# Kernel optimization log

Measured on AMD Instinct MI355X. Metric: run time of the kernel, lower is better.

The kernel has to match this reference:

```python
import jax, jax.numpy as jnp
import numpy as np

ALPHA = 2.0   # spikingjelly surrogate.ATan default alpha
TAU = 2.0
VTH = 1.0
EPS = 1e-5

@jax.custom_vjp
def atan_spike(x):
    return (x >= 0.0).astype(x.dtype)

def _as_fwd(x):
    return atan_spike(x), x

def _as_bwd(x, g):
    # ATan surrogate derivative: alpha/2 / (1 + (pi/2*alpha*x)^2)
    return (g * (ALPHA / 2.0) / (1.0 + (jnp.pi / 2.0 * ALPHA * x) ** 2),)

atan_spike.defvjp(_as_fwd, _as_bwd)

def lif_multistep(x):
    # x: [B, T, D]; LIF with decay_input=True, v_reset=0 (hard reset), detach_reset=True
    xt = jnp.swapaxes(x, 0, 1)  # [T, B, D] time-major
    def step(v, xi):
        v = v + (xi - v) / TAU                       # integrate with input decay
        s = atan_spike(v - VTH)                       # fire (surrogate grad)
        v = v * (1.0 - jax.lax.stop_gradient(s))      # hard reset to 0, detached
        return v, s
    _, spikes = jax.lax.scan(step, jnp.zeros_like(xt[0]), xt)
    return jnp.swapaxes(spikes, 0, 1)  # [B, T, D]

def layernorm(x, g, b):
    m = x.mean(-1, keepdims=True)
    v = x.var(-1, keepdims=True)
    return (x - m) / jnp.sqrt(v + EPS) * g + b

def setup_inputs() -> dict:
    key = jax.random.key(0)
    ks = jax.random.split(key, 6)
    B, T, IN, HP, E, H, D = 256, 256, 4, 64, 512, 1024, 4
    s = 0.02
    return {
        "hist_feat": jax.random.normal(ks[0], (B, T, IN), jnp.float32),
        "pW1": jax.random.normal(ks[1], (IN, HP), jnp.float32) * s,
        "pb1": jnp.zeros((HP,), jnp.float32),
        "pW2": jax.random.normal(ks[2], (HP, E), jnp.float32) * s,
        "pb2": jnp.zeros((E,), jnp.float32),
        "fc1_w": jax.random.normal(ks[3], (D, E, H), jnp.float32) * s,
        "fc1_b": jnp.zeros((D, H), jnp.float32),
        "ln1_g": jnp.ones((D, H), jnp.float32),
        "ln1_b": jnp.zeros((D, H), jnp.float32),
        "fc2_w": jax.random.normal(ks[4], (D, H, E), jnp.float32) * s,
        "fc2_b": jnp.zeros((D, E), jnp.float32),
        "ln2_g": jnp.ones((D, E), jnp.float32),
        "ln2_b": jnp.zeros((D, E), jnp.float32),
    }

def reference(hist_feat, pW1, pb1, pW2, pb2, fc1_w, fc1_b, ln1_g, ln1_b,
              fc2_w, fc2_b, ln2_g, ln2_b):
    # input projector: Linear -> exact GELU -> Linear
    x = jax.nn.gelu(hist_feat @ pW1 + pb1, approximate=False) @ pW2 + pb2  # [B,T,E]
    depth = fc1_w.shape[0]
    for d in range(depth):  # small fixed layer loop
        res = x
        h = layernorm(x @ fc1_w[d] + fc1_b[d], ln1_g[d], ln1_b[d])  # [B,T,H]
        h = lif_multistep(h)
        h = layernorm(h @ fc2_w[d] + fc2_b[d], ln2_g[d], ln2_b[d])  # [B,T,E]
        h = lif_multistep(h)
        x = res + h  # dropout is identity in eval mode
    return x[:, -1]  # pooling='last', no mask -> last timestep, [B,E]
```

## Files before the change

### kernel.cpp

```cpp
#include <hip/hip_runtime.h>
#include <hip/hip_bf16.h>
#include <math.h>

#define B_  256
#define T_  256
#define IN_ 4
#define HP_ 64
#define E_  512
#define H_  1024
#define D_  4

typedef __hip_bfloat16 bf16;
typedef _Float16 f16;
typedef _Float16 f16x8 __attribute__((ext_vector_type(8)));
typedef float f32x4 __attribute__((ext_vector_type(4)));

__device__ __forceinline__ float load1(const void* p, size_t idx, bool isb) {
    if (isb) {
        unsigned int u = ((const unsigned short*)p)[idx];
        return __uint_as_float(u << 16);
    }
    return ((const float*)p)[idx];
}

__device__ __forceinline__ float4 load4(const void* p, size_t idx, bool isb) {
    if (isb) {
        ushort4 u = *(const ushort4*)((const unsigned short*)p + idx);
        float4 r;
        r.x = __uint_as_float(((unsigned int)u.x) << 16);
        r.y = __uint_as_float(((unsigned int)u.y) << 16);
        r.z = __uint_as_float(((unsigned int)u.z) << 16);
        r.w = __uint_as_float(((unsigned int)u.w) << 16);
        return r;
    }
    return *((const float4*)p + (idx >> 2));
}

__device__ __forceinline__ void split3(float x, f16& h, f16& hs, f16& lb) {
    h = (f16)x;
    float hf = (float)h;
    hs = (f16)(hf * 4.8828125e-4f);
    lb = (f16)((x - hf) * 2048.0f);
}

__global__ void sniff_count_kernel(const unsigned short* __restrict__ p,
                                   int* __restrict__ cnts) {
    __shared__ int cnt;
    if (threadIdx.x == 0) cnt = 0;
    __syncthreads();
    int local = 0;
    #pragma unroll
    for (int k = 0; k < 4; ++k) {
        int i = blockIdx.x * 1024 + k * 256 + threadIdx.x;
        unsigned int bits = ((unsigned int)p[i]) << 16;
        float v = __uint_as_float(bits);
        float a = fabsf(v);
        if (!(a <= 1e4f)) local++;
        else if (v != 0.0f && a < 1e-6f) local++;
    }
    atomicAdd(&cnt, local);
    __syncthreads();
    if (threadIdx.x == 0) cnts[blockIdx.x] = cnt;
}

__global__ void sniff_final_kernel(const int* __restrict__ cnts,
                                   int* __restrict__ flag) {
    int s = 0;
    for (int i = 0; i < 64; ++i) s += cnts[i];
    *flag = (s > 1024) ? 0 : 1;
}

__global__ __launch_bounds__(256) void wsplit_kernel(
        const void* __restrict__ W, size_t wOff, unsigned short* __restrict__ Wt,
        int K, int N, const int* __restrict__ flag) {
    const bool isb = (*flag != 0);
    __shared__ float tile[32][33];
    const int n0 = blockIdx.x * 32, k0 = blockIdx.y * 32;
    const int t = threadIdx.x;
    {
        int lk = t >> 3, ln0 = (t & 7) << 2;
        float4 v = load4(W, wOff + (size_t)(k0 + lk) * N + n0 + ln0, isb);
        tile[lk][ln0 + 0] = v.x; tile[lk][ln0 + 1] = v.y;
        tile[lk][ln0 + 2] = v.z; tile[lk][ln0 + 3] = v.w;
    }
    __syncthreads();
    int n = t >> 3, kq0 = (t & 7) << 2;
    size_t base = (size_t)(n0 + n) * (2 * (size_t)K) + k0 + kq0;
    #pragma unroll
    for (int j = 0; j < 4; ++j) {
        float x = tile[kq0 + j][n];
        f16 h, hs, lb;
        split3(x, h, hs, lb);
        Wt[base + j]     = *(unsigned short*)&h;
        Wt[base + j + K] = *(unsigned short*)&lb;
    }
}

template<int NPL>
__device__ __forceinline__ void gemm_mfma_body(
        const unsigned short* __restrict__ At, const unsigned short* __restrict__ Wt,
        const void* __restrict__ bias, size_t bOff,
        float* __restrict__ C, int N, int K, const int* __restrict__ flag) {
    const bool isb = (*flag != 0);
    constexpr int APL = (NPL == 3) ? 2 : 1;
    __shared__ unsigned short As[2][128 * 64];
    __shared__ unsigned short Bs[2][128 * 64];

    const int gx = N >> 7;
    const int gy = (int)gridDim.x / gx;
    int bx, by;
    {
        int bid = blockIdx.x;
        if ((gy & 7) == 0) {
            int k = bid & 7, i = bid >> 3;
            bx = i % gx;
            by = (gy >> 3) * k + i / gx;
        } else { bx = bid % gx; by = bid / gx; }
    }
    const int bn = bx * 128;
    const int bm = by * 128;

    const int tid  = threadIdx.x;
    const int lane = tid & 63;
    const int wave = tid >> 6;
    const int wm = wave >> 1;
    const int wn = wave & 1;
    const int g  = lane >> 4;
    const int lr = lane & 15;

    const int sar = tid >> 1;
    const int sah = tid & 1;
    const int sbn = tid >> 1;
    const int sq  = tid & 1;

    const f16 C11 = (f16)4.8828125e-4f;
    const f16x8 c11v = {C11, C11, C11, C11, C11, C11, C11, C11};

    f32x4 acc[4][4];
    #pragma unroll
    for (int i = 0; i < 4; ++i)
        #pragma unroll
        for (int j = 0; j < 4; ++j) acc[i][j] = (f32x4){0.f, 0.f, 0.f, 0.f};

    const unsigned short* Ap = At + (size_t)(bm + sar) * (APL * (size_t)K) + sah * 16;
    const unsigned short* Wp = Wt + (size_t)(bn + sbn) * (2 * (size_t)K) + sq * 16;

    f16x8 av[2 * APL], wv[4];
    #pragma unroll
    for (int pl = 0; pl < APL; ++pl)
        #pragma unroll
        for (int c = 0; c < 2; ++c)
            av[pl * 2 + c] = *(const f16x8*)(Ap + (size_t)pl * K + c * 8);
    #pragma unroll
    for (int pl = 0; pl < 2; ++pl)
        #pragma unroll
        for (int c = 0; c < 2; ++c)
            wv[pl * 2 + c] = *(const f16x8*)(Wp + (size_t)pl * K + c * 8);

    const int nt = K >> 5;
    for (int t = 0; t < nt; ++t) {
        const int cur = t & 1;
        const int arb = sar * 64, asw = sar & 7;
        #pragma unroll
        for (int pl = 0; pl < APL; ++pl)
            #pragma unroll
            for (int c = 0; c < 2; ++c) {
                const int gg = sah * 2 + c;
                *(f16x8*)&As[cur][arb + (((pl << 2) | gg) ^ asw) * 8] = av[pl * 2 + c];
            }
        const int brb = sbn * 64, bsw = sbn & 7;
        #pragma unroll
        for (int pl = 0; pl < 2; ++pl)
            #pragma unroll
            for (int c = 0; c < 2; ++c) {
                const int gg = sq * 2 + c;
                *(f16x8*)&Bs[cur][brb + (((pl << 2) | gg) ^ bsw) * 8] = wv[pl * 2 + c];
            }
        __syncthreads();
        if (t + 1 < nt) {
            const int k0 = (t + 1) << 5;
            #pragma unroll
            for (int pl = 0; pl < APL; ++pl)
                #pragma unroll
                for (int c = 0; c < 2; ++c)
                    av[pl * 2 + c] = *(const f16x8*)(Ap + (size_t)pl * K + k0 + c * 8);
            #pragma unroll
            for (int pl = 0; pl < 2; ++pl)
                #pragma unroll
                for (int c = 0; c < 2; ++c)
                    wv[pl * 2 + c] = *(const f16x8*)(Wp + (size_t)pl * K + k0 + c * 8);
        }
        f16x8 a0[4], b0[4], b2[4], a2[4];
        #pragma unroll
        for (int mi = 0; mi < 4; ++mi) {
            const int ar = wm * 64 + mi * 16 + lr;
            a0[mi] = *(const f16x8*)&As[cur][ar * 64 + ((g ^ (ar & 7))) * 8];
            if (NPL == 3)
                a2[mi] = *(const f16x8*)&As[cur][ar * 64 + (((4 | g) ^ (ar & 7))) * 8];
        }
        #pragma unroll
        for (int ni = 0; ni < 4; ++ni) {
            const int br = wn * 64 + ni * 16 + lr;
            b0[ni] = *(const f16x8*)&Bs[cur][br * 64 + ((g ^ (br & 7))) * 8];
            b2[ni] = *(const f16x8*)&Bs[cur][br * 64 + (((4 | g) ^ (br & 7))) * 8];
        }
        #pragma unroll
        for (int mi = 0; mi < 4; ++mi)
            #pragma unroll
            for (int ni = 0; ni < 4; ++ni)
                acc[mi][ni] = __builtin_amdgcn_mfma_f32_16x16x32_f16(
                    a0[mi], b0[ni], acc[mi][ni], 0, 0, 0);
        {
            f16x8 a1[4];
            #pragma unroll
            for (int mi = 0; mi < 4; ++mi) a1[mi] = a0[mi] * c11v;
            #pragma unroll
            for (int mi = 0; mi < 4; ++mi)
                #pragma unroll
                for (int ni = 0; ni < 4; ++ni)
                    acc[mi][ni] = __builtin_amdgcn_mfma_f32_16x16x32_f16(
                        a1[mi], b2[ni], acc[mi][ni], 0, 0, 0);
        }
        if (NPL == 3) {
            f16x8 b1[4];
            #pragma unroll
            for (int ni = 0; ni < 4; ++ni) b1[ni] = b0[ni] * c11v;
            #pragma unroll
            for (int mi = 0; mi < 4; ++mi)
                #pragma unroll
                for (int ni = 0; ni < 4; ++ni)
                    acc[mi][ni] = __builtin_amdgcn_mfma_f32_16x16x32_f16(
                        a2[mi], b1[ni], acc[mi][ni], 0, 0, 0);
        }
    }
    #pragma unroll
    for (int ni = 0; ni < 4; ++ni) {
        const int col = bn + wn * 64 + ni * 16 + lr;
        const float bv = load1(bias, bOff + col, isb);
        #pragma unroll
        for (int mi = 0; mi < 4; ++mi) {
            #pragma unroll
            for (int r = 0; r < 4; ++r) {
                const size_t row = (size_t)(bm + wm * 64 + mi * 16 + g * 4 + r);
                C[row * N + col] = acc[mi][ni][r] + bv;
            }
        }
    }
}

__global__ __launch_bounds__(256, 3) void gemm_mfma3_kernel(
        const unsigned short* __restrict__ At, const unsigned short* __restrict__ Wt,
        const void* __restrict__ bias, size_t bOff,
        float* __restrict__ C, int N, int K, const int* __restrict__ flag) {
    gemm_mfma_body<3>(At, Wt, bias, bOff, C, N, K, flag);
}

__global__ __launch_bounds__(256, 3) void gemm_mfma2_kernel(
        const unsigned short* __restrict__ At, const unsigned short* __restrict__ Wt,
        const void* __restrict__ bias, size_t bOff,
        float* __restrict__ C, int N, int K, const int* __restrict__ flag) {
    gemm_mfma_body<2>(At, Wt, bias, bOff, C, N, K, flag);
}

#define RB_ 16
__global__ __launch_bounds__(256) void proj_kernel(
        const void* __restrict__ hist, const void* __restrict__ pW1,
        const void* __restrict__ pb1,  const void* __restrict__ pW2,
        const void* __restrict__ pb2,  float* __restrict__ Xc,
        unsigned short* __restrict__ At1,
        size_t m0, const int* __restrict__ flag) {
    const bool isb = (*flag != 0);
    __shared__ float h1[RB_][HP_];
    const size_t mb = (size_t)blockIdx.x * RB_;
    const int tid = threadIdx.x;
    const int lane = tid & 63;
    const int grp = tid >> 6;
    #pragma unroll
    for (int rep = 0; rep < 4; ++rep) {
        int idx = tid + rep * 256;
        int r = idx >> 6, c = idx & 63;
        size_t gm = m0 + mb + r;
        float acc = 0.f;
        #pragma unroll
        for (int i = 0; i < IN_; ++i)
            acc = fmaf(load1(hist, gm * IN_ + i, isb),
                       load1(pW1, (size_t)i * HP_ + c, isb), acc);
        acc += load1(pb1, c, isb);
        h1[r][c] = 0.5f * acc * (1.0f + erff(acc * 0.70710678118654752440f));
    }
    __syncthreads();
    const int e0 = lane * 8;
    float acc[4][8];
    #pragma unroll
    for (int r = 0; r < 4; ++r)
        #pragma unroll
        for (int j = 0; j < 8; ++j) acc[r][j] = 0.f;
    for (int i = 0; i < HP_; ++i) {
        float4 wA = load4(pW2, (size_t)i * E_ + e0, isb);
        float4 wB = load4(pW2, (size_t)i * E_ + e0 + 4, isb);
        float w[8] = {wA.x, wA.y, wA.z, wA.w, wB.x, wB.y, wB.z, wB.w};
        #pragma unroll
        for (int r = 0; r < 4; ++r) {
            float h = h1[grp * 4 + r][i];
            #pragma unroll
            for (int j = 0; j < 8; ++j) acc[r][j] = fmaf(h, w[j], acc[r][j]);
        }
    }
    #pragma unroll
    for (int r = 0; r < 4; ++r) {
        size_t row = mb + grp * 4 + r;
        float o[8];
        #pragma unroll
        for (int j = 0; j < 8; ++j)
            o[j] = acc[r][j] + load1(pb2, e0 + j, isb);
        *(float4*)(Xc + row * E_ + e0)     = (float4){o[0], o[1], o[2], o[3]};
        *(float4*)(Xc + row * E_ + e0 + 4) = (float4){o[4], o[5], o[6], o[7]};
        f16x8 hv, lv;
        #pragma unroll
        for (int j = 0; j < 8; ++j) {
            f16 h, hs, lb;
            split3(o[j], h, hs, lb);
            hv[j] = h; lv[j] = lb;
        }
        *(f16x8*)&At1[row * (2 * E_) + e0]      = hv;
        *(f16x8*)&At1[row * (2 * E_) + E_ + e0] = lv;
    }
}

__device__ __forceinline__ float block_sum(float v, float* smem, int tid) {
    #pragma unroll
    for (int off = 32; off > 0; off >>= 1) v += __shfl_down(v, off, 64);
    __syncthreads();
    if ((tid & 63) == 0) smem[tid >> 6] = v;
    __syncthreads();
    if (tid == 0) smem[4] = smem[0] + smem[1] + smem[2] + smem[3];
    __syncthreads();
    return smem[4];
}

__global__ __launch_bounds__(256) void ln_stats_kernel(const float* __restrict__ Y,
                                                       float* __restrict__ stats,
                                                       int N) {
    __shared__ float smem[5];
    size_t row = blockIdx.x;
    const float* y = Y + row * (size_t)N;
    int tid = threadIdx.x;
    int nPer = N >> 8;
    float vals[4];
    float s = 0.f;
    for (int i = 0; i < nPer; ++i) { float v = y[tid + (i << 8)]; vals[i] = v; s += v; }
    float mean = block_sum(s, smem, tid) / (float)N;
    float sq = 0.f;
    for (int i = 0; i < nPer; ++i) { float d0 = vals[i] - mean; sq += d0 * d0; }
    float var = block_sum(sq, smem, tid) / (float)N;
    if (tid == 0) {
        stats[row * 2]     = mean;
        stats[row * 2 + 1] = sqrtf(var + 1e-5f);
    }
}

__global__ __launch_bounds__(64) void lif_kernel(const float* __restrict__ Y,
                                                 const float* __restrict__ stats,
                                                 const void* __restrict__ g, size_t gOff,
                                                 const void* __restrict__ b, size_t bOff,
                                                 unsigned short* __restrict__ At2,
                                                 int N, const int* __restrict__ flag) {
    const bool isb = (*flag != 0);
    int f = blockIdx.x * 64 + threadIdx.x;
    int bb = blockIdx.y;
    const float gw = load1(g, gOff + f, isb);
    const float bw = load1(b, bOff + f, isb);
    size_t base = (size_t)bb * T_ * N + f;
    size_t srow = (size_t)bb * T_;
    float v = 0.f;
    for (int t0 = 0; t0 < T_; t0 += 16) {
        float x[16], mn[16], dn[16], s[16];
        #pragma unroll
        for (int j = 0; j < 16; ++j) {
            x[j]  = Y[base + (size_t)(t0 + j) * N];
            mn[j] = stats[(srow + t0 + j) * 2];
            dn[j] = stats[(srow + t0 + j) * 2 + 1];
        }
        #pragma unroll
        for (int j = 0; j < 16; ++j) {
            float xn = (x[j] - mn[j]) / dn[j] * gw + bw;
            v = v + (xn - v) * 0.5f;
            s[j] = (v - 1.0f >= 0.0f) ? 1.0f : 0.0f;
            v = v * (1.0f - s[j]);
        }
        #pragma unroll
        for (int j = 0; j < 16; ++j) {
            f16 h = (f16)s[j];
            At2[base + (size_t)(t0 + j) * N] = *(unsigned short*)&h;
        }
    }
}

__global__ __launch_bounds__(64) void lif_add_kernel(const float* __restrict__ Z,
                                                     const float* __restrict__ stats,
                                                     const void* __restrict__ g, size_t gOff,
                                                     const void* __restrict__ b, size_t bOff,
                                                     float* __restrict__ Xc,
                                                     unsigned short* __restrict__ At1,
                                                     void* __restrict__ outp, int b0,
                                                     int lastLayer,
                                                     const int* __restrict__ flag) {
    const bool isb = (*flag != 0);
    int e = blockIdx.x * 64 + threadIdx.x;
    int bb = blockIdx.y;
    const float gw = load1(g, gOff + e, isb);
    const float bw = load1(b, bOff + e, isb);
    size_t base  = (size_t)bb * T_ * E_ + e;
    size_t base2 = (size_t)bb * T_ * (2 * E_) + e;
    size_t srow  = (size_t)bb * T_;
    float v = 0.f;
    for (int t0 = 0; t0 < T_; t0 += 16) {
        float x[16], xc[16], mn[16], dn[16], s[16];
        #pragma unroll
        for (int j = 0; j < 16; ++j) {
            x[j]  = Z[base + (size_t)(t0 + j) * E_];
            mn[j] = stats[(srow + t0 + j) * 2];
            dn[j] = stats[(srow + t0 + j) * 2 + 1];
        }
        #pragma unroll
        for (int j = 0; j < 16; ++j) xc[j] = Xc[base + (size_t)(t0 + j) * E_];
        #pragma unroll
        for (int j = 0; j < 16; ++j) {
            float xn = (x[j] - mn[j]) / dn[j] * gw + bw;
            v = v + (xn - v) * 0.5f;
            s[j] = (v - 1.0f >= 0.0f) ? 1.0f : 0.0f;
            v = v * (1.0f - s[j]);
        }
        #pragma unroll
        for (int j = 0; j < 16; ++j) {
            float nx = xc[j] + s[j];
            Xc[base + (size_t)(t0 + j) * E_] = nx;
            f16 h, hs, lb;
            split3(nx, h, hs, lb);
            At1[base2 + (size_t)(t0 + j) * (2 * E_)]      = *(unsigned short*)&h;
            At1[base2 + (size_t)(t0 + j) * (2 * E_) + E_] = *(unsigned short*)&lb;
        }
        if (lastLayer && t0 + 16 == T_) {
            float nx = Xc[base + (size_t)(T_ - 1) * E_];
            size_t oi = (size_t)(b0 + bb) * E_ + e;
            if (isb) ((bf16*)outp)[oi] = __float2bfloat16(nx);
            else     ((float*)outp)[oi] = nx;
        }
    }
}

extern "C" void kernel_launch(void* const* d_in, const int* in_sizes, int n_in,
                              void* d_out, int out_size, void* d_ws, size_t ws_size,
                              hipStream_t stream) {
    char* ws = (char*)d_ws;
    int* flag = (int*)ws;
    int* cnts = (int*)(ws + 64);

    const size_t wtCount = 2 * (size_t)E_ * H_;
    const size_t wtBytes = 2 * D_ * wtCount * sizeof(unsigned short);
    unsigned short* Wt1 = (unsigned short*)(ws + 512);
    unsigned short* Wt2 = Wt1 + (size_t)D_ * wtCount;

    size_t used = 512 + wtBytes;
    size_t avail = (ws_size > used) ? ws_size - used : 0;
    const size_t perBatch = (size_t)T_ * ((E_ + H_ + E_) * 4 + 2 * E_ * 2 + H_ * 2 + 16);
    int CB = 256;
    while (CB > 1 && (size_t)CB * perBatch > avail) CB >>= 1;
    const int R = CB * T_;

    float* Xc  = (float*)(ws + used);
    float* HBc = Xc + (size_t)R * E_;
    float* Y2c = HBc + (size_t)R * H_;
    unsigned short* At1 = (unsigned short*)(Y2c + (size_t)R * E_);
    unsigned short* At2 = At1 + (size_t)R * 2 * E_;
    float* St1 = (float*)(At2 + (size_t)R * H_);
    float* St2 = St1 + (size_t)R * 2;

    sniff_count_kernel<<<64, 256, 0, stream>>>((const unsigned short*)d_in[0], cnts);
    sniff_final_kernel<<<1, 1, 0, stream>>>(cnts, flag);

    for (int d = 0; d < D_; ++d) {
        wsplit_kernel<<<dim3(H_ / 32, E_ / 32), 256, 0, stream>>>(
            d_in[5], (size_t)d * E_ * H_, Wt1 + (size_t)d * wtCount, E_, H_, flag);
        wsplit_kernel<<<dim3(E_ / 32, H_ / 32), 256, 0, stream>>>(
            d_in[9], (size_t)d * H_ * E_, Wt2 + (size_t)d * wtCount, H_, E_, flag);
    }

    for (int b0 = 0; b0 < B_; b0 += CB) {
        proj_kernel<<<R / RB_, 256, 0, stream>>>(d_in[0], d_in[1], d_in[2], d_in[3],
                                                 d_in[4], Xc, At1, (size_t)b0 * T_, flag);
        for (int d = 0; d < D_; ++d) {
            size_t b1o = (size_t)d * H_;
            size_t b2o = (size_t)d * E_;

            gemm_mfma3_kernel<<<(H_ / 128) * (R / 128), 256, 0, stream>>>(
                At1, Wt1 + (size_t)d * wtCount, d_in[6], b1o, HBc, H_, E_, flag);
            ln_stats_kernel<<<R, 256, 0, stream>>>(HBc, St1, H_);
            lif_kernel<<<dim3(H_ / 64, CB), 64, 0, stream>>>(
                HBc, St1, d_in[7], b1o, d_in[8], b1o, At2, H_, flag);

            gemm_mfma2_kernel<<<(E_ / 128) * (R / 128), 256, 0, stream>>>(
                At2, Wt2 + (size_t)d * wtCount, d_in[10], b2o, Y2c, E_, H_, flag);
            ln_stats_kernel<<<R, 256, 0, stream>>>(Y2c, St2, E_);
            lif_add_kernel<<<dim3(E_ / 64, CB), 64, 0, stream>>>(
                Y2c, St2, d_in[11], b2o, d_in[12], b2o, Xc, At1,
                d_out, b0, (d == D_ - 1) ? 1 : 0, flag);
        }
    }
}
```

Measured before the change: 3.354 ms.

## Split fc1 GEMM into dedicated 512-thread kernel with single-buffered LDS

The three-pass split-f16 GEMM for fc1 becomes its own kernel launched with 512 threads (8 waves, each owning a 32x64 sub-tile instead of 64x64), halving per-wave accumulator registers. Its LDS staging drops from double to single buffering, with a second barrier per k-step. The fc2 GEMM is specialized into a separate two-pass kernel with the unused a2 path removed. The aim is more waves in flight to hide latency in the fc1 GEMM, at the cost of extra synchronization and less load/compute overlap.

Result: slower. 3.437 ms (+2.5%).

```diff
diff --git a/kernel.cpp b/kernel.cpp
--- a/kernel.cpp
+++ b/kernel.cpp
@@ -96,15 +96,13 @@
     }
 }
 
-template<int NPL>
-__device__ __forceinline__ void gemm_mfma_body(
+__global__ __launch_bounds__(512, 2) void gemm_mfma3_kernel(
         const unsigned short* __restrict__ At, const unsigned short* __restrict__ Wt,
         const void* __restrict__ bias, size_t bOff,
         float* __restrict__ C, int N, int K, const int* __restrict__ flag) {
     const bool isb = (*flag != 0);
-    constexpr int APL = (NPL == 3) ? 2 : 1;
-    __shared__ unsigned short As[2][128 * 64];
-    __shared__ unsigned short Bs[2][128 * 64];
+    __shared__ unsigned short As[128 * 64];
+    __shared__ unsigned short Bs[128 * 64];
 
     const int gx = N >> 7;
     const int gy = (int)gridDim.x / gx;
@@ -128,6 +126,129 @@
     const int g  = lane >> 4;
     const int lr = lane & 15;
 
+    const int sar = tid >> 2;
+    const int skq = tid & 3;
+
+    const f16 C11 = (f16)4.8828125e-4f;
+    const f16x8 c11v = {C11, C11, C11, C11, C11, C11, C11, C11};
+
+    f32x4 acc[2][4];
+    #pragma unroll
+    for (int i = 0; i < 2; ++i)
+        #pragma unroll
+        for (int j = 0; j < 4; ++j) acc[i][j] = (f32x4){0.f, 0.f, 0.f, 0.f};
+
+    const unsigned short* Ap = At + (size_t)(bm + sar) * (2 * (size_t)K) + skq * 8;
+    const unsigned short* Wp = Wt + (size_t)(bn + sar) * (2 * (size_t)K) + skq * 8;
+
+    f16x8 av0 = *(const f16x8*)(Ap);
+    f16x8 av1 = *(const f16x8*)(Ap + K);
+    f16x8 wv0 = *(const f16x8*)(Wp);
+    f16x8 wv1 = *(const f16x8*)(Wp + K);
+
+    const int nt = K >> 5;
+    for (int t = 0; t < nt; ++t) {
+        const int arb = sar * 64, asw = sar & 7;
+        *(f16x8*)&As[arb + ((skq ^ asw)) * 8]       = av0;
+        *(f16x8*)&As[arb + (((4 | skq) ^ asw)) * 8] = av1;
+        *(f16x8*)&Bs[arb + ((skq ^ asw)) * 8]       = wv0;
+        *(f16x8*)&Bs[arb + (((4 | skq) ^ asw)) * 8] = wv1;
+        __syncthreads();
+        if (t + 1 < nt) {
+            const int k0 = (t + 1) << 5;
+            av0 = *(const f16x8*)(Ap + k0);
+            av1 = *(const f16x8*)(Ap + K + k0);
+            wv0 = *(const f16x8*)(Wp + k0);
+            wv1 = *(const f16x8*)(Wp + K + k0);
+        }
+        f16x8 a0[2], a2[2], b0[4], b2[4];
+        #pragma unroll
+        for (int mi = 0; mi < 2; ++mi) {
+            const int ar = wm * 32 + mi * 16 + lr;
+            a0[mi] = *(const f16x8*)&As[ar * 64 + ((g ^ (ar & 7))) * 8];
+            a2[mi] = *(const f16x8*)&As[ar * 64 + (((4 | g) ^ (ar & 7))) * 8];
+        }
+        #pragma unroll
+        for (int ni = 0; ni < 4; ++ni) {
+            const int br = wn * 64 + ni * 16 + lr;
+            b0[ni] = *(const f16x8*)&Bs[br * 64 + ((g ^ (br & 7))) * 8];
+            b2[ni] = *(const f16x8*)&Bs[br * 64 + (((4 | g) ^ (br & 7))) * 8];
+        }
+        #pragma unroll
+        for (int mi = 0; mi < 2; ++mi)
+            #pragma unroll
+            for (int ni = 0; ni < 4; ++ni)
+                acc[mi][ni] = __builtin_amdgcn_mfma_f32_16x16x32_f16(
+                    a0[mi], b0[ni], acc[mi][ni], 0, 0, 0);
+        {
+            f16x8 a1[2];
+            #pragma unroll
+            for (int mi = 0; mi < 2; ++mi) a1[mi] = a0[mi] * c11v;
+            #pragma unroll
+            for (int mi = 0; mi < 2; ++mi)
+                #pragma unroll
+                for (int ni = 0; ni < 4; ++ni)
+                    acc[mi][ni] = __builtin_amdgcn_mfma_f32_16x16x32_f16(
+                        a1[mi], b2[ni], acc[mi][ni], 0, 0, 0);
+        }
+        {
+            f16x8 b1[4];
+            #pragma unroll
+            for (int ni = 0; ni < 4; ++ni) b1[ni] = b0[ni] * c11v;
+            #pragma unroll
+            for (int mi = 0; mi < 2; ++mi)
+                #pragma unroll
+                for (int ni = 0; ni < 4; ++ni)
+                    acc[mi][ni] = __builtin_amdgcn_mfma_f32_16x16x32_f16(
+                        a2[mi], b1[ni], acc[mi][ni], 0, 0, 0);
+        }
+        __syncthreads();
+    }
+    #pragma unroll
+    for (int ni = 0; ni < 4; ++ni) {
+        const int col = bn + wn * 64 + ni * 16 + lr;
+        const float bv = load1(bias, bOff + col, isb);
+        #pragma unroll
+        for (int mi = 0; mi < 2; ++mi) {
+            #pragma unroll
+            for (int r = 0; r < 4; ++r) {
+                const size_t row = (size_t)(bm + wm * 32 + mi * 16 + g * 4 + r);
+                C[row * N + col] = acc[mi][ni][r] + bv;
+            }
+        }
+    }
+}
+
+__global__ __launch_bounds__(256, 3) void gemm_mfma2_kernel(
+        const unsigned short* __restrict__ At, const unsigned short* __restrict__ Wt,
+        const void* __restrict__ bias, size_t bOff,
+        float* __restrict__ C, int N, int K, const int* __restrict__ flag) {
+    const bool isb = (*flag != 0);
+    __shared__ unsigned short As[2][128 * 64];
+    __shared__ unsigned short Bs[2][128 * 64];
+
+    const int gx = N >> 7;
+    const int gy = (int)gridDim.x / gx;
+    int bx, by;
+    {
+        int bid = blockIdx.x;
+        if ((gy & 7) == 0) {
+            int k = bid & 7, i = bid >> 3;
+            bx = i % gx;
+            by = (gy >> 3) * k + i / gx;
+        } else { bx = bid % gx; by = bid / gx; }
+    }
+    const int bn = bx * 128;
+    const int bm = by * 128;
+
+    const int tid  = threadIdx.x;
+    const int lane = tid & 63;
+    const int wave = tid >> 6;
+    const int wm = wave >> 1;
+    const int wn = wave & 1;
+    const int g  = lane >> 4;
+    const int lr = lane & 15;
+
     const int sar = tid >> 1;
     const int sah = tid & 1;
     const int sbn = tid >> 1;
@@ -142,15 +263,13 @@
         #pragma unroll
         for (int j = 0; j < 4; ++j) acc[i][j] = (f32x4){0.f, 0.f, 0.f, 0.f};
 
-    const unsigned short* Ap = At + (size_t)(bm + sar) * (APL * (size_t)K) + sah * 16;
+    const unsigned short* Ap = At + (size_t)(bm + sar) * (size_t)K + sah * 16;
     const unsigned short* Wp = Wt + (size_t)(bn + sbn) * (2 * (size_t)K) + sq * 16;
 
-    f16x8 av[2 * APL], wv[4];
-    #pragma unroll
-    for (int pl = 0; pl < APL; ++pl)
-        #pragma unroll
-        for (int c = 0; c < 2; ++c)
-            av[pl * 2 + c] = *(const f16x8*)(Ap + (size_t)pl * K + c * 8);
+    f16x8 av[2], wv[4];
+    #pragma unroll
+    for (int c = 0; c < 2; ++c)
+        av[c] = *(const f16x8*)(Ap + c * 8);
     #pragma unroll
     for (int pl = 0; pl < 2; ++pl)
         #pragma unroll
@@ -162,12 +281,10 @@
         const int cur = t & 1;
         const int arb = sar * 64, asw = sar & 7;
         #pragma unroll
-        for (int pl = 0; pl < APL; ++pl)
-            #pragma unroll
-            for (int c = 0; c < 2; ++c) {
-                const int gg = sah * 2 + c;
-                *(f16x8*)&As[cur][arb + (((pl << 2) | gg) ^ asw) * 8] = av[pl * 2 + c];
-            }
+        for (int c = 0; c < 2; ++c) {
+            const int gg = sah * 2 + c;
+            *(f16x8*)&As[cur][arb + ((gg ^ asw)) * 8] = av[c];
+        }
         const int brb = sbn * 64, bsw = sbn & 7;
         #pragma unroll
         for (int pl = 0; pl < 2; ++pl)
@@ -180,23 +297,19 @@
         if (t + 1 < nt) {
             const int k0 = (t + 1) << 5;
             #pragma unroll
-            for (int pl = 0; pl < APL; ++pl)
-                #pragma unroll
-                for (int c = 0; c < 2; ++c)
-                    av[pl * 2 + c] = *(const f16x8*)(Ap + (size_t)pl * K + k0 + c * 8);
+            for (int c = 0; c < 2; ++c)
+                av[c] = *(const f16x8*)(Ap + k0 + c * 8);
             #pragma unroll
             for (int pl = 0; pl < 2; ++pl)
                 #pragma unroll
                 for (int c = 0; c < 2; ++c)
                     wv[pl * 2 + c] = *(const f16x8*)(Wp + (size_t)pl * K + k0 + c * 8);
         }
-        f16x8 a0[4], b0[4], b2[4], a2[4];
+        f16x8 a0[4], b0[4], b2[4];
         #pragma unroll
         for (int mi = 0; mi < 4; ++mi) {
             const int ar = wm * 64 + mi * 16 + lr;
             a0[mi] = *(const f16x8*)&As[cur][ar * 64 + ((g ^ (ar & 7))) * 8];
-            if (NPL == 3)
-                a2[mi] = *(const f16x8*)&As[cur][ar * 64 + (((4 | g) ^ (ar & 7))) * 8];
         }
         #pragma unroll
         for (int ni = 0; ni < 4; ++ni) {
@@ -221,17 +334,6 @@
                     acc[mi][ni] = __builtin_amdgcn_mfma_f32_16x16x32_f16(
                         a1[mi], b2[ni], acc[mi][ni], 0, 0, 0);
         }
-        if (NPL == 3) {
-            f16x8 b1[4];
-            #pragma unroll
-            for (int ni = 0; ni < 4; ++ni) b1[ni] = b0[ni] * c11v;
-            #pragma unroll
-            for (int mi = 0; mi < 4; ++mi)
-                #pragma unroll
-                for (int ni = 0; ni < 4; ++ni)
-                    acc[mi][ni] = __builtin_amdgcn_mfma_f32_16x16x32_f16(
-                        a2[mi], b1[ni], acc[mi][ni], 0, 0, 0);
-        }
     }
     #pragma unroll
     for (int ni = 0; ni < 4; ++ni) {
@@ -246,20 +348,6 @@
             }
         }
     }
-}
-
-__global__ __launch_bounds__(256, 3) void gemm_mfma3_kernel(
-        const unsigned short* __restrict__ At, const unsigned short* __restrict__ Wt,
-        const void* __restrict__ bias, size_t bOff,
-        float* __restrict__ C, int N, int K, const int* __restrict__ flag) {
-    gemm_mfma_body<3>(At, Wt, bias, bOff, C, N, K, flag);
-}
-
-__global__ __launch_bounds__(256, 3) void gemm_mfma2_kernel(
-        const unsigned short* __restrict__ At, const unsigned short* __restrict__ Wt,
-        const void* __restrict__ bias, size_t bOff,
-        float* __restrict__ C, int N, int K, const int* __restrict__ flag) {
-    gemm_mfma_body<2>(At, Wt, bias, bOff, C, N, K, flag);
 }
 
 #define RB_ 16
@@ -493,7 +581,7 @@
             size_t b1o = (size_t)d * H_;
             size_t b2o = (size_t)d * E_;
 
-            gemm_mfma3_kernel<<<(H_ / 128) * (R / 128), 256, 0, stream>>>(
+            gemm_mfma3_kernel<<<(H_ / 128) * (R / 128), 512, 0, stream>>>(
                 At1, Wt1 + (size_t)d * wtCount, d_in[6], b1o, HBc, H_, E_, flag);
             ln_stats_kernel<<<R, 256, 0, stream>>>(HBc, St1, H_);
             lif_kernel<<<dim3(H_ / 64, CB), 64, 0, stream>>>(
```
